# Optimization experiments

Measured on AMD Instinct MI355X. Metric: run time of the kernel, lower is better.

## Reference

```python
import jax, jax.numpy as jnp
import numpy as np
import math

B, T, D = 2, 4096, 1024
P, H, NH = 16, 64, 16  # prototypes, head_dim, num_heads
EPS = 1e-6
GAIN = 1.0
STD = 0.02

def setup_inputs() -> dict:
    key = jax.random.key(0)
    ks = jax.random.split(key, 8)
    hidden_states = jax.random.normal(ks[0], (B, T, D), jnp.float32)
    # rotary embeddings (standard HF RoPE, theta=10000)
    inv_freq = 1.0 / (10000.0 ** (np.arange(0, H, 2, dtype=np.float32) / H))
    t = np.arange(T, dtype=np.float32)
    freqs = np.outer(t, inv_freq)                     # [T, H/2]
    emb = np.concatenate([freqs, freqs], axis=-1)     # [T, H]
    cos = jnp.broadcast_to(jnp.cos(emb)[None], (B, T, H)).astype(jnp.float32)
    sin = jnp.broadcast_to(jnp.sin(emb)[None], (B, T, H)).astype(jnp.float32)
    return {
        'hidden_states': hidden_states,
        'cos': cos, 'sin': sin,
        'q_norm_w': jnp.ones((D,), jnp.float32),
        'k_proto': STD * jax.random.normal(ks[1], (P, D), jnp.float32),
        'v_proto': jnp.eye(P, dtype=jnp.float32),     # nn.init.eye_
        'q_basis': STD * jax.random.normal(ks[2], (P, D, H), jnp.float32),
        'k_basis': STD * jax.random.normal(ks[3], (P, D, H), jnp.float32),
        'v_basis': STD * jax.random.normal(ks[4], (P, D, H), jnp.float32),
        'o_w': STD * jax.random.normal(ks[5], (D, NH * H), jnp.float32),  # o_proj weight [out,in]
    }

def _rms_norm(x, w, eps=EPS):
    xf = x.astype(jnp.float32)
    var = jnp.mean(xf * xf, axis=-1, keepdims=True)
    return (xf * jax.lax.rsqrt(var + eps)).astype(x.dtype) * w

def _rotate_half(x):
    x1, x2 = jnp.split(x, 2, axis=-1)
    return jnp.concatenate([-x2, x1], axis=-1)

def reference(hidden_states, cos, sin, q_norm_w, k_proto, v_proto, q_basis, k_basis, v_basis, o_w):
    x = hidden_states
    # CAPR router
    q_r = _rms_norm(x, q_norm_w)
    aw = jax.nn.softmax(jnp.einsum('btd,pd->btp', q_r, k_proto) / math.sqrt(D), axis=-1)
    routing = jax.nn.softmax(jnp.einsum('btp,pq->btq', aw, v_proto) * GAIN, axis=-1)  # [B,T,P]
    # per-prototype projections then routing-weighted reduction over P
    # (same math as einsum('btp,pdh,btd->bth'), avoids [B,T,D,H] intermediate)
    def proj(basis):
        xp = jnp.einsum('btd,pdh->btph', x, basis)        # [B,T,P,H]
        return jnp.einsum('btp,btph->bth', routing, xp)   # [B,T,H]
    q, k, v = proj(q_basis), proj(k_basis), proj(v_basis)
    # RoPE (all num_heads copies are identical, so operate on the single head)
    q = q * cos + _rotate_half(q) * sin
    k = k * cos + _rotate_half(k) * sin
    # causal SDPA, scale = 1/sqrt(head_dim)
    scores = jnp.einsum('bqh,bkh->bqk', q, k) / math.sqrt(H)
    causal = jnp.tril(jnp.ones((T, T), bool))
    scores = jnp.where(causal[None], scores, jnp.finfo(scores.dtype).min)
    probs = jax.nn.softmax(scores, axis=-1)
    attn = jnp.einsum('bqk,bkh->bqh', probs, v)           # [B,T,H]
    # heads are expanded copies -> concat is a tile; then o_proj (no bias)
    concat = jnp.tile(attn, (1, 1, NH))                   # [B,T,NH*H]
    out = jnp.einsum('bti,oi->bto', concat, o_w)
    return out
```

## Files before the change

kernel.cpp:

```cpp
#include <hip/hip_runtime.h>

typedef __attribute__((ext_vector_type(8))) short bf16x8;
typedef __attribute__((ext_vector_type(4))) float f32x4;
typedef __attribute__((ext_vector_type(4))) unsigned short us4;

#define DEV __device__ __forceinline__

static constexpr int Bn = 2, Tn = 4096, Dn = 1024, Pn = 16, Hn = 64;
static constexpr int BT = Bn * Tn;
static constexpr int NC = 3 * Dn;
static constexpr int NUNIT = 288;

static constexpr size_t OFF_ROUTING = 0;
static constexpr size_t OFF_XBF     = OFF_ROUTING + (size_t)BT * 16 * 4;
static constexpr size_t OFF_BPK     = OFF_XBF + (size_t)BT * Dn * 2;
static constexpr size_t OFF_QKV     = OFF_BPK + (size_t)NC * Dn * 2;
static constexpr size_t OFF_QBF     = OFF_QKV + (size_t)BT * 192 * 4;
static constexpr size_t OFF_KBF     = OFF_QBF + (size_t)BT * 64 * 2;
static constexpr size_t OFF_VT      = OFF_KBF + (size_t)BT * 64 * 2;
static constexpr size_t OFF_ATTNB   = OFF_VT + (size_t)BT * 64 * 2;
static constexpr size_t OFF_OWEFF   = OFF_ATTNB + (size_t)BT * 64 * 2;

DEV unsigned short f2bf(float f) {
  unsigned int u = __builtin_bit_cast(unsigned int, f);
  u += 0x7fffu + ((u >> 16) & 1u);
  return (unsigned short)(u >> 16);
}

DEV unsigned int cvtpk(float a, float b) {
  unsigned int r;
  asm("v_cvt_pk_bf16_f32 %0, %1, %2" : "=v"(r) : "v"(a), "v"(b));
  return r;
}

DEV void gll16(const void* g, void* l) {
  __builtin_amdgcn_global_load_lds(
      (const __attribute__((address_space(1))) void*)g,
      (__attribute__((address_space(3))) void*)l, 16, 0, 0);
}

__global__ __launch_bounds__(256)
void router_kernel(const float* __restrict__ x, const float* __restrict__ w,
                   const float* __restrict__ kproto, const float* __restrict__ vproto,
                   float* __restrict__ routing, unsigned short* __restrict__ xbf)
{
  __shared__ float lgs[8][16];
  const int tid = threadIdx.x, wid = tid >> 6, lane = tid & 63;
  const int t0 = blockIdx.x * 8;

  float wv[16];
#pragma unroll
  for (int c = 0; c < 4; ++c) {
    float4 f = *(const float4*)(w + c * 256 + lane * 4);
    wv[c*4+0] = f.x; wv[c*4+1] = f.y; wv[c*4+2] = f.z; wv[c*4+3] = f.w;
  }

  float xr[2][16];
  float rs[2];
#pragma unroll
  for (int rr = 0; rr < 2; ++rr) {
    const int row = t0 + wid * 2 + rr;
    float ss = 0.f;
#pragma unroll
    for (int c = 0; c < 4; ++c) {
      float4 f = *(const float4*)(x + (size_t)row * 1024 + c * 256 + lane * 4);
      xr[rr][c*4+0] = f.x; xr[rr][c*4+1] = f.y; xr[rr][c*4+2] = f.z; xr[rr][c*4+3] = f.w;
      ss += f.x*f.x + f.y*f.y + f.z*f.z + f.w*f.w;
      us4 o; o[0] = f2bf(f.x); o[1] = f2bf(f.y); o[2] = f2bf(f.z); o[3] = f2bf(f.w);
      *(us4*)(xbf + (size_t)row * 1024 + c * 256 + lane * 4) = o;
    }
#pragma unroll
    for (int off = 1; off < 64; off <<= 1) ss += __shfl_xor(ss, off, 64);
    rs[rr] = rsqrtf(ss * (1.f / 1024.f) + 1e-6f);
  }

  for (int p = 0; p < 16; ++p) {
    float d0 = 0.f, d1 = 0.f;
#pragma unroll
    for (int c = 0; c < 4; ++c) {
      float4 f = *(const float4*)(kproto + (size_t)p * 1024 + c * 256 + lane * 4);
      float k0 = f.x * wv[c*4+0], k1 = f.y * wv[c*4+1], k2 = f.z * wv[c*4+2], k3 = f.w * wv[c*4+3];
      d0 += xr[0][c*4+0]*k0 + xr[0][c*4+1]*k1 + xr[0][c*4+2]*k2 + xr[0][c*4+3]*k3;
      d1 += xr[1][c*4+0]*k0 + xr[1][c*4+1]*k1 + xr[1][c*4+2]*k2 + xr[1][c*4+3]*k3;
    }
#pragma unroll
    for (int off = 1; off < 64; off <<= 1) {
      d0 += __shfl_xor(d0, off, 64);
      d1 += __shfl_xor(d1, off, 64);
    }
    if (lane == 0) {
      lgs[wid*2+0][p] = d0 * rs[0] * 0.03125f;
      lgs[wid*2+1][p] = d1 * rs[1] * 0.03125f;
    }
  }
  __syncthreads();
  if (tid < 8) {
    float lg[16];
#pragma unroll
    for (int p = 0; p < 16; ++p) lg[p] = lgs[tid][p];
    float m = -1e30f;
#pragma unroll
    for (int p = 0; p < 16; ++p) m = fmaxf(m, lg[p]);
    float aw[16]; float s = 0.f;
#pragma unroll
    for (int p = 0; p < 16; ++p) { aw[p] = __expf(lg[p] - m); s += aw[p]; }
    float inv = 1.f / s;
    float rt[16];
#pragma unroll
    for (int q = 0; q < 16; ++q) {
      float a = 0.f;
#pragma unroll
      for (int p = 0; p < 16; ++p) a += aw[p] * vproto[p * 16 + q];
      rt[q] = a * inv;
    }
    float m2 = -1e30f;
#pragma unroll
    for (int q = 0; q < 16; ++q) m2 = fmaxf(m2, rt[q]);
    float e[16]; float s2 = 0.f;
#pragma unroll
    for (int q = 0; q < 16; ++q) { e[q] = __expf(rt[q] - m2); s2 += e[q]; }
    float inv2 = 1.f / s2;
#pragma unroll
    for (int q = 0; q < 16; ++q) routing[(size_t)(t0 + tid) * 16 + q] = e[q] * inv2;
  }
}

__global__ __launch_bounds__(256)
void pack_bases_kernel(const float* __restrict__ qb, const float* __restrict__ kb,
                       const float* __restrict__ vb, unsigned short* __restrict__ bpk)
{
  __shared__ float tile[64][65];
  const int bid = blockIdx.x;
  const int bs = bid >> 8;
  const int p = (bid >> 4) & 15;
  const int dt = bid & 15;
  const float* src = bs == 0 ? qb : (bs == 1 ? kb : vb);
  const int tid = threadIdx.x;
#pragma unroll
  for (int j = 0; j < 4; ++j) {
    int slot = tid + j * 256;
    int r = slot >> 4;
    int c4 = slot & 15;
    float4 v = *(const float4*)(src + (size_t)p * 65536 + (size_t)(dt * 64 + r) * 64 + c4 * 4);
    tile[r][c4*4+0] = v.x; tile[r][c4*4+1] = v.y; tile[r][c4*4+2] = v.z; tile[r][c4*4+3] = v.w;
  }
  __syncthreads();
#pragma unroll
  for (int j = 0; j < 4; ++j) {
    int slot = tid + j * 256;
    int h = slot >> 4;
    int d4 = slot & 15;
    us4 o;
    o[0] = f2bf(tile[d4*4+0][h]); o[1] = f2bf(tile[d4*4+1][h]);
    o[2] = f2bf(tile[d4*4+2][h]); o[3] = f2bf(tile[d4*4+3][h]);
    int c = bs * 1024 + h * 16 + p;
    *(us4*)(bpk + (size_t)c * 1024 + dt * 64 + d4 * 4) = o;
  }
}

__global__ __launch_bounds__(256)
void pack_ow_kernel(const float* __restrict__ ow, unsigned short* __restrict__ oweff)
{
  int idx = blockIdx.x * 256 + threadIdx.x;
  int o = idx >> 6, h = idx & 63;
  float s = 0.f;
#pragma unroll
  for (int n = 0; n < 16; ++n) s += ow[(size_t)o * 1024 + n * 64 + h];
  oweff[idx] = f2bf(s);
}

__global__ __launch_bounds__(256)
void proj_gemm_kernel(const unsigned short* __restrict__ bpk,
                      const unsigned short* __restrict__ xbf,
                      const float* __restrict__ routing,
                      float* __restrict__ qkv)
{
  __shared__ __attribute__((aligned(16))) unsigned short As[2][128][64];
  __shared__ __attribute__((aligned(16))) unsigned short Bs[2][128][64];
  const int bid = blockIdx.x;
  const int swz = (bid & 7) * 192 + (bid >> 3);
  const int tt = swz / 24, ct = swz - tt * 24;
  const int c0 = ct << 7, t0 = tt << 7;
  const int tid = threadIdx.x, wid = tid >> 6, lane = tid & 63;
  const int wm = (wid >> 1) << 6, wn = (wid & 1) << 6;
  const int l15 = lane & 15, l4 = lane >> 4;
  const int sx = (l15 & 7) << 3;

  f32x4 acc[4][4];
#pragma unroll
  for (int m = 0; m < 4; ++m)
#pragma unroll
    for (int n = 0; n < 4; ++n) acc[m][n] = (f32x4){0.f, 0.f, 0.f, 0.f};

#define PROJ_STAGE(kt, pb) do {                                              \
    const int k0_ = (kt) * 64;                                               \
    const int cc_ = 8 * ((lane & 7) ^ (lane >> 3));  \
    _Pragma("unroll")                                                        \
    for (int i_ = 0; i_ < 4; ++i_) {                                         \
      int ch_ = wid * 4 + i_;                                                \
      int r_ = ch_ * 8 + (lane >> 3);                                        \
      gll16(bpk + (size_t)(c0 + r_) * 1024 + k0_ + cc_, &As[pb][ch_ * 8][0]);\
      gll16(xbf + (size_t)(t0 + r_) * 1024 + k0_ + cc_, &Bs[pb][ch_ * 8][0]);\
    } } while (0)

  PROJ_STAGE(0, 0);
  PROJ_STAGE(1, 1);

  for (int kt = 0; kt < 16; ++kt) {
    const int cb = kt & 1;
    if (kt < 15) asm volatile("s_waitcnt vmcnt(8)" ::: "memory");
    else         asm volatile("s_waitcnt vmcnt(0)" ::: "memory");
    asm volatile("s_barrier" ::: "memory");
#pragma unroll
    for (int kk = 0; kk < 2; ++kk) {
      bf16x8 af[4], bfr[4];
#pragma unroll
      for (int m = 0; m < 4; ++m)
        af[m] = *(const bf16x8*)&As[cb][wm + m * 16 + l15][(kk * 32 + l4 * 8) ^ sx];
#pragma unroll
      for (int n = 0; n < 4; ++n)
        bfr[n] = *(const bf16x8*)&Bs[cb][wn + n * 16 + l15][(kk * 32 + l4 * 8) ^ sx];
#pragma unroll
      for (int m = 0; m < 4; ++m)
#pragma unroll
        for (int n = 0; n < 4; ++n)
          acc[m][n] = __builtin_amdgcn_mfma_f32_16x16x32_bf16(af[m], bfr[n], acc[m][n], 0, 0, 0);
    }
    asm volatile("s_waitcnt lgkmcnt(0)" ::: "memory");
    asm volatile("s_barrier" ::: "memory");
    if (kt < 14) PROJ_STAGE(kt + 2, cb);
  }
#undef PROJ_STAGE

#pragma unroll
  for (int n = 0; n < 4; ++n) {
    const int t = t0 + wn + n * 16 + l15;
    const float4 rt = *(const float4*)(routing + (size_t)t * 16 + l4 * 4);
#pragma unroll
    for (int m = 0; m < 4; ++m) {
      float s = acc[m][n][0] * rt.x + acc[m][n][1] * rt.y
              + acc[m][n][2] * rt.z + acc[m][n][3] * rt.w;
      s += __shfl_xor(s, 16, 64);
      s += __shfl_xor(s, 32, 64);
      if (l4 == 0) {
        const int h16 = (c0 + wm + m * 16) >> 4;
        qkv[(size_t)t * 192 + h16] = s;
      }
    }
  }
}

__global__ __launch_bounds__(256)
void rope_kernel(const float* __restrict__ qkv, const float* __restrict__ cosb,
                 const float* __restrict__ sinb, unsigned short* __restrict__ qbf,
                 unsigned short* __restrict__ kbf, unsigned short* __restrict__ vT)
{
  constexpr float QS = 0.125f * 1.4426950408889634f;
  __shared__ float vs[64][33];
  const int tid = threadIdx.x;
  const int bt0 = blockIdx.x * 32;
  const int tokl = tid >> 3;
  const int h0 = (tid & 7) * 4;
  const size_t bt = bt0 + tokl;
  const float* base = qkv + bt * 192;
  float4 q1 = *(const float4*)(base + h0);
  float4 q2 = *(const float4*)(base + h0 + 32);
  float4 k1 = *(const float4*)(base + 64 + h0);
  float4 k2 = *(const float4*)(base + 64 + h0 + 32);
  float4 v1 = *(const float4*)(base + 128 + h0);
  float4 v2 = *(const float4*)(base + 128 + h0 + 32);
  const float* cp = cosb + bt * 64;
  const float* sp = sinb + bt * 64;
  float4 c1 = *(const float4*)(cp + h0), c2 = *(const float4*)(cp + h0 + 32);
  float4 s1 = *(const float4*)(sp + h0), s2 = *(const float4*)(sp + h0 + 32);

  us4 uq1, uq2, uk1, uk2;
  uq1[0] = f2bf((q1.x * c1.x - q2.x * s1.x) * QS);
  uq1[1] = f2bf((q1.y * c1.y - q2.y * s1.y) * QS);
  uq1[2] = f2bf((q1.z * c1.z - q2.z * s1.z) * QS);
  uq1[3] = f2bf((q1.w * c1.w - q2.w * s1.w) * QS);
  uq2[0] = f2bf((q2.x * c2.x + q1.x * s2.x) * QS);
  uq2[1] = f2bf((q2.y * c2.y + q1.y * s2.y) * QS);
  uq2[2] = f2bf((q2.z * c2.z + q1.z * s2.z) * QS);
  uq2[3] = f2bf((q2.w * c2.w + q1.w * s2.w) * QS);
  uk1[0] = f2bf(k1.x * c1.x - k2.x * s1.x);
  uk1[1] = f2bf(k1.y * c1.y - k2.y * s1.y);
  uk1[2] = f2bf(k1.z * c1.z - k2.z * s1.z);
  uk1[3] = f2bf(k1.w * c1.w - k2.w * s1.w);
  uk2[0] = f2bf(k2.x * c2.x + k1.x * s2.x);
  uk2[1] = f2bf(k2.y * c2.y + k1.y * s2.y);
  uk2[2] = f2bf(k2.z * c2.z + k1.z * s2.z);
  uk2[3] = f2bf(k2.w * c2.w + k1.w * s2.w);
  *(us4*)(qbf + bt * 64 + h0) = uq1;
  *(us4*)(qbf + bt * 64 + h0 + 32) = uq2;
  *(us4*)(kbf + bt * 64 + h0) = uk1;
  *(us4*)(kbf + bt * 64 + h0 + 32) = uk2;

  vs[h0 + 0][tokl] = v1.x; vs[h0 + 1][tokl] = v1.y; vs[h0 + 2][tokl] = v1.z; vs[h0 + 3][tokl] = v1.w;
  vs[h0 + 32][tokl] = v2.x; vs[h0 + 33][tokl] = v2.y; vs[h0 + 34][tokl] = v2.z; vs[h0 + 35][tokl] = v2.w;
  __syncthreads();
  const int h = tid >> 2, c8 = (tid & 3) * 8;
  const int b = bt0 >> 12, tb0 = bt0 & 4095;
  us4 o0, o1;
  o0[0] = f2bf(vs[h][c8 + 0]); o0[1] = f2bf(vs[h][c8 + 1]);
  o0[2] = f2bf(vs[h][c8 + 2]); o0[3] = f2bf(vs[h][c8 + 3]);
  o1[0] = f2bf(vs[h][c8 + 4]); o1[1] = f2bf(vs[h][c8 + 5]);
  o1[2] = f2bf(vs[h][c8 + 6]); o1[3] = f2bf(vs[h][c8 + 7]);
  unsigned short* vp = vT + ((size_t)b * 64 + h) * 4096 + tb0 + c8;
  *(us4*)vp = o0;
  *(us4*)(vp + 4) = o1;
}

__global__ __launch_bounds__(256)
void attn_kernel(const unsigned short* __restrict__ qbf,
                 const unsigned short* __restrict__ kbf,
                 const unsigned short* __restrict__ vT,
                 float* __restrict__ po, float* __restrict__ ml)
{
  const int bid = blockIdx.x;
  const int b = bid / NUNIT, u = bid - b * NUNIT;
  int g = 0;
  while (u >= 4 * (g + 1) * (g + 2)) ++g;
  const int r0 = u - 4 * g * (g + 1);
  const int qq = r0 / (g + 1);
  const int qt = 8 * g + qq;
  const int c = r0 - qq * (g + 1);
  const int ks = c * 512;
  const int ke = min(ks + 512, (qt + 1) * 64);

  const int tid = threadIdx.x, w = tid >> 6, lane = tid & 63;
  const int l15 = lane & 15, l4 = lane >> 4;
  const int q0w = qt * 64 + w * 16;
  const int qg = q0w + l15;

  const unsigned short* qp = qbf + (size_t)(b * 4096 + qg) * 64 + l4 * 8;
  bf16x8 qf0 = *(const bf16x8*)qp;
  bf16x8 qf1 = *(const bf16x8*)(qp + 32);

  f32x4 oacc[4];
#pragma unroll
  for (int hf = 0; hf < 4; ++hf) oacc[hf] = (f32x4){0.f, 0.f, 0.f, 0.f};
  float m = -1e30f, l = 0.f;

  const int kew = min(ke, q0w + 16);
  const int nst = (kew - ks + 63) >> 6;
  const int kperm = 8 * (l15 >> 2) + (l15 & 3);

  for (int st = 0; st < nst; ++st) {
    const int key0 = ks + st * 64;
    f32x4 s[4];
#pragma unroll
    for (int j = 0; j < 4; ++j) {
      const int krow = key0 + 32 * (j >> 1) + 4 * (j & 1) + kperm;
      const unsigned short* kp = kbf + (size_t)(b * 4096 + krow) * 64 + l4 * 8;
      bf16x8 ka = *(const bf16x8*)kp;
      bf16x8 kc = *(const bf16x8*)(kp + 32);
      f32x4 z = (f32x4){0.f, 0.f, 0.f, 0.f};
      z = __builtin_amdgcn_mfma_f32_16x16x32_bf16(ka, qf0, z, 0, 0, 0);
      s[j] = __builtin_amdgcn_mfma_f32_16x16x32_bf16(kc, qf1, z, 0, 0, 0);
    }
    bf16x8 vf[4][2];
#pragma unroll
    for (int J = 0; J < 2; ++J)
#pragma unroll
      for (int hf = 0; hf < 4; ++hf)
        vf[hf][J] = *(const bf16x8*)(vT + ((size_t)(b * 64 + hf * 16 + l15)) * 4096
                                     + key0 + J * 32 + l4 * 8);
    if (key0 + 63 > q0w) {
#pragma unroll
      for (int j = 0; j < 4; ++j) {
        const int kb0 = key0 + 32 * (j >> 1) + 4 * (j & 1) + 8 * l4;
#pragma unroll
        for (int rr = 0; rr < 4; ++rr)
          if (kb0 + rr > qg) s[j][rr] = -1e30f;
      }
    }
    float pmax = -1e30f;
#pragma unroll
    for (int j = 0; j < 4; ++j)
#pragma unroll
      for (int rr = 0; rr < 4; ++rr) pmax = fmaxf(pmax, s[j][rr]);
    pmax = fmaxf(pmax, __shfl_xor(pmax, 16, 64));
    pmax = fmaxf(pmax, __shfl_xor(pmax, 32, 64));
    const float mn = fmaxf(m, pmax);
    const float sc = __builtin_amdgcn_exp2f(m - mn);
    m = mn;
    l *= sc;
#pragma unroll
    for (int hf = 0; hf < 4; ++hf) {
      oacc[hf][0] *= sc; oacc[hf][1] *= sc; oacc[hf][2] *= sc; oacc[hf][3] *= sc;
    }
    float rs = 0.f;
    unsigned int cvw[4][2];
#pragma unroll
    for (int j = 0; j < 4; ++j) {
      const float e0 = (s[j][0] > -1e29f) ? __builtin_amdgcn_exp2f(s[j][0] - m) : 0.f;
      const float e1 = (s[j][1] > -1e29f) ? __builtin_amdgcn_exp2f(s[j][1] - m) : 0.f;
      const float e2 = (s[j][2] > -1e29f) ? __builtin_amdgcn_exp2f(s[j][2] - m) : 0.f;
      const float e3 = (s[j][3] > -1e29f) ? __builtin_amdgcn_exp2f(s[j][3] - m) : 0.f;
      rs += (e0 + e1) + (e2 + e3);
      cvw[j][0] = cvtpk(e0, e1);
      cvw[j][1] = cvtpk(e2, e3);
    }
    rs += __shfl_xor(rs, 16, 64);
    rs += __shfl_xor(rs, 32, 64);
    l += rs;
#pragma unroll
    for (int J = 0; J < 2; ++J) {
      union { unsigned int uu[4]; bf16x8 v; } pk;
      pk.uu[0] = cvw[2 * J][0];
      pk.uu[1] = cvw[2 * J][1];
      pk.uu[2] = cvw[2 * J + 1][0];
      pk.uu[3] = cvw[2 * J + 1][1];
#pragma unroll
      for (int hf = 0; hf < 4; ++hf)
        oacc[hf] = __builtin_amdgcn_mfma_f32_16x16x32_bf16(vf[hf][J], pk.v, oacc[hf], 0, 0, 0);
    }
  }

  const size_t ug = (size_t)b * NUNIT + u;
  float* pop = po + (ug * 64 + w * 16 + l15) * 64;
#pragma unroll
  for (int hf = 0; hf < 4; ++hf)
    *(f32x4*)(pop + hf * 16 + l4 * 4) = oacc[hf];
  if (l4 == 0) {
    ml[ug * 128 + w * 16 + l15] = m;
    ml[ug * 128 + 64 + w * 16 + l15] = l;
  }
}

__global__ __launch_bounds__(256)
void combine_kernel(const float* __restrict__ po, const float* __restrict__ ml,
                    unsigned short* __restrict__ attnb)
{
  const int bid = blockIdx.x;
  const int b = bid >> 6, qt = bid & 63;
  const int g = qt >> 3, r = qt & 7;
  const int nch = g + 1;
  const size_t ub = (size_t)b * NUNIT + (size_t)(g + 1) * (4 * g + r);
  const int tid = threadIdx.x;
  const int q = tid >> 2, hc = (tid & 3) * 16;

  float mt = -1e30f;
  for (int i = 0; i < nch; ++i) mt = fmaxf(mt, ml[(ub + i) * 128 + q]);
  float lt = 0.f;
  float4 a0 = {0,0,0,0}, a1 = {0,0,0,0}, a2 = {0,0,0,0}, a3 = {0,0,0,0};
  for (int i = 0; i < nch; ++i) {
    const float mi = ml[(ub + i) * 128 + q];
    const float wi = (mi > -1e29f) ? __builtin_amdgcn_exp2f(mi - mt) : 0.f;
    lt += wi * ml[(ub + i) * 128 + 64 + q];
    const float* pp = po + ((ub + i) * 64 + q) * 64 + hc;
    float4 f0 = *(const float4*)(pp + 0);
    float4 f1 = *(const float4*)(pp + 4);
    float4 f2 = *(const float4*)(pp + 8);
    float4 f3 = *(const float4*)(pp + 12);
    a0.x += wi * f0.x; a0.y += wi * f0.y; a0.z += wi * f0.z; a0.w += wi * f0.w;
    a1.x += wi * f1.x; a1.y += wi * f1.y; a1.z += wi * f1.z; a1.w += wi * f1.w;
    a2.x += wi * f2.x; a2.y += wi * f2.y; a2.z += wi * f2.z; a2.w += wi * f2.w;
    a3.x += wi * f3.x; a3.y += wi * f3.y; a3.z += wi * f3.z; a3.w += wi * f3.w;
  }
  const float inv = (lt > 0.f) ? 1.f / lt : 0.f;
  unsigned short* op = attnb + ((size_t)b * 4096 + qt * 64 + q) * 64 + hc;
  us4 o;
  o[0] = f2bf(a0.x * inv); o[1] = f2bf(a0.y * inv); o[2] = f2bf(a0.z * inv); o[3] = f2bf(a0.w * inv);
  *(us4*)(op + 0) = o;
  o[0] = f2bf(a1.x * inv); o[1] = f2bf(a1.y * inv); o[2] = f2bf(a1.z * inv); o[3] = f2bf(a1.w * inv);
  *(us4*)(op + 4) = o;
  o[0] = f2bf(a2.x * inv); o[1] = f2bf(a2.y * inv); o[2] = f2bf(a2.z * inv); o[3] = f2bf(a2.w * inv);
  *(us4*)(op + 8) = o;
  o[0] = f2bf(a3.x * inv); o[1] = f2bf(a3.y * inv); o[2] = f2bf(a3.z * inv); o[3] = f2bf(a3.w * inv);
  *(us4*)(op + 12) = o;
}

__global__ __launch_bounds__(256)
void oproj_kernel(const unsigned short* __restrict__ attnb,
                  const unsigned short* __restrict__ oweff,
                  float* __restrict__ out)
{
  __shared__ __attribute__((aligned(16))) unsigned short As[128][64];
  __shared__ __attribute__((aligned(16))) unsigned short Bs[128][64];
  const int bid = blockIdx.x;
  const int swz = (bid & 7) * 64 + (bid >> 3);
  const int mt = swz >> 3, nt = swz & 7;
  const int m0 = mt << 7, n0 = nt << 7;
  const int tid = threadIdx.x, wid = tid >> 6, lane = tid & 63;
  const int wm = (wid >> 1) << 6, wn = (wid & 1) << 6;
  const int l15 = lane & 15, l4 = lane >> 4;

#pragma unroll
  for (int i = 0; i < 4; ++i) {
    int ch = wid * 4 + i;
    int r = ch * 8 + (lane >> 3), c = (lane & 7) * 8;
    gll16(attnb + (size_t)(m0 + r) * 64 + c, &As[ch * 8][0]);
    gll16(oweff + (size_t)(n0 + r) * 64 + c, &Bs[ch * 8][0]);
  }
  __syncthreads();

  f32x4 acc[4][4];
#pragma unroll
  for (int m = 0; m < 4; ++m)
#pragma unroll
    for (int n = 0; n < 4; ++n) acc[m][n] = (f32x4){0.f, 0.f, 0.f, 0.f};
#pragma unroll
  for (int kk = 0; kk < 2; ++kk) {
    bf16x8 af[4], bfr[4];
#pragma unroll
    for (int m = 0; m < 4; ++m) af[m] = *(const bf16x8*)&As[wm + m * 16 + l15][kk * 32 + l4 * 8];
#pragma unroll
    for (int n = 0; n < 4; ++n) bfr[n] = *(const bf16x8*)&Bs[wn + n * 16 + l15][kk * 32 + l4 * 8];
#pragma unroll
    for (int m = 0; m < 4; ++m)
#pragma unroll
      for (int n = 0; n < 4; ++n)
        acc[m][n] = __builtin_amdgcn_mfma_f32_16x16x32_bf16(af[m], bfr[n], acc[m][n], 0, 0, 0);
  }
#pragma unroll
  for (int m = 0; m < 4; ++m)
#pragma unroll
    for (int n = 0; n < 4; ++n)
#pragma unroll
      for (int r = 0; r < 4; ++r)
        out[(size_t)(m0 + wm + m * 16 + l4 * 4 + r) * 1024 + n0 + wn + n * 16 + l15] = acc[m][n][r];
}

extern "C" void kernel_launch(void* const* d_in, const int* in_sizes, int n_in,
                              void* d_out, int out_size, void* d_ws, size_t ws_size,
                              hipStream_t stream) {
  const float* x      = (const float*)d_in[0];
  const float* cosb   = (const float*)d_in[1];
  const float* sinb   = (const float*)d_in[2];
  const float* qw     = (const float*)d_in[3];
  const float* kproto = (const float*)d_in[4];
  const float* vproto = (const float*)d_in[5];
  const float* qb     = (const float*)d_in[6];
  const float* kb     = (const float*)d_in[7];
  const float* vb     = (const float*)d_in[8];
  const float* ow     = (const float*)d_in[9];
  float* out = (float*)d_out;
  char* ws = (char*)d_ws;

  float* routing        = (float*)(ws + OFF_ROUTING);
  unsigned short* xbf   = (unsigned short*)(ws + OFF_XBF);
  unsigned short* bpk   = (unsigned short*)(ws + OFF_BPK);
  float* qkv            = (float*)(ws + OFF_QKV);
  unsigned short* qbf   = (unsigned short*)(ws + OFF_QBF);
  unsigned short* kbf   = (unsigned short*)(ws + OFF_KBF);
  unsigned short* vT    = (unsigned short*)(ws + OFF_VT);
  unsigned short* attnb = (unsigned short*)(ws + OFF_ATTNB);
  unsigned short* oweff = (unsigned short*)(ws + OFF_OWEFF);
  float* po             = (float*)(ws + OFF_XBF);
  float* ml             = (float*)(ws + OFF_BPK);

  router_kernel<<<BT / 8, 256, 0, stream>>>(x, qw, kproto, vproto, routing, xbf);
  pack_bases_kernel<<<768, 256, 0, stream>>>(qb, kb, vb, bpk);
  pack_ow_kernel<<<256, 256, 0, stream>>>(ow, oweff);
  proj_gemm_kernel<<<1536, 256, 0, stream>>>(bpk, xbf, routing, qkv);
  rope_kernel<<<BT / 32, 256, 0, stream>>>(qkv, cosb, sinb, qbf, kbf, vT);
  attn_kernel<<<Bn * NUNIT, 256, 0, stream>>>(qbf, kbf, vT, po, ml);
  combine_kernel<<<128, 256, 0, stream>>>(po, ml, attnb);
  oproj_kernel<<<512, 256, 0, stream>>>(attnb, oweff, out);
}
```

Before: 152.0 us.

## Merge prep kernels and enlarge projection GEMM tile with triple buffering

```diff
diff --git a/kernel.cpp b/kernel.cpp
--- a/kernel.cpp
+++ b/kernel.cpp
@@ -40,151 +40,152 @@
 }
 
 __global__ __launch_bounds__(256)
-void router_kernel(const float* __restrict__ x, const float* __restrict__ w,
-                   const float* __restrict__ kproto, const float* __restrict__ vproto,
-                   float* __restrict__ routing, unsigned short* __restrict__ xbf)
+void prep_kernel(const float* __restrict__ x, const float* __restrict__ w,
+                 const float* __restrict__ kproto, const float* __restrict__ vproto,
+                 const float* __restrict__ qb, const float* __restrict__ kb,
+                 const float* __restrict__ vb, const float* __restrict__ ow,
+                 float* __restrict__ routing, unsigned short* __restrict__ xbf,
+                 unsigned short* __restrict__ bpk, unsigned short* __restrict__ oweff)
 {
   __shared__ float lgs[8][16];
-  const int tid = threadIdx.x, wid = tid >> 6, lane = tid & 63;
-  const int t0 = blockIdx.x * 8;
-
-  float wv[16];
-#pragma unroll
-  for (int c = 0; c < 4; ++c) {
-    float4 f = *(const float4*)(w + c * 256 + lane * 4);
-    wv[c*4+0] = f.x; wv[c*4+1] = f.y; wv[c*4+2] = f.z; wv[c*4+3] = f.w;
-  }
-
-  float xr[2][16];
-  float rs[2];
-#pragma unroll
-  for (int rr = 0; rr < 2; ++rr) {
-    const int row = t0 + wid * 2 + rr;
-    float ss = 0.f;
-#pragma unroll
-    for (int c = 0; c < 4; ++c) {
-      float4 f = *(const float4*)(x + (size_t)row * 1024 + c * 256 + lane * 4);
-      xr[rr][c*4+0] = f.x; xr[rr][c*4+1] = f.y; xr[rr][c*4+2] = f.z; xr[rr][c*4+3] = f.w;
-      ss += f.x*f.x + f.y*f.y + f.z*f.z + f.w*f.w;
-      us4 o; o[0] = f2bf(f.x); o[1] = f2bf(f.y); o[2] = f2bf(f.z); o[3] = f2bf(f.w);
-      *(us4*)(xbf + (size_t)row * 1024 + c * 256 + lane * 4) = o;
-    }
-#pragma unroll
-    for (int off = 1; off < 64; off <<= 1) ss += __shfl_xor(ss, off, 64);
-    rs[rr] = rsqrtf(ss * (1.f / 1024.f) + 1e-6f);
-  }
-
-  for (int p = 0; p < 16; ++p) {
-    float d0 = 0.f, d1 = 0.f;
-#pragma unroll
-    for (int c = 0; c < 4; ++c) {
-      float4 f = *(const float4*)(kproto + (size_t)p * 1024 + c * 256 + lane * 4);
-      float k0 = f.x * wv[c*4+0], k1 = f.y * wv[c*4+1], k2 = f.z * wv[c*4+2], k3 = f.w * wv[c*4+3];
-      d0 += xr[0][c*4+0]*k0 + xr[0][c*4+1]*k1 + xr[0][c*4+2]*k2 + xr[0][c*4+3]*k3;
-      d1 += xr[1][c*4+0]*k0 + xr[1][c*4+1]*k1 + xr[1][c*4+2]*k2 + xr[1][c*4+3]*k3;
-    }
-#pragma unroll
-    for (int off = 1; off < 64; off <<= 1) {
-      d0 += __shfl_xor(d0, off, 64);
-      d1 += __shfl_xor(d1, off, 64);
-    }
-    if (lane == 0) {
-      lgs[wid*2+0][p] = d0 * rs[0] * 0.03125f;
-      lgs[wid*2+1][p] = d1 * rs[1] * 0.03125f;
-    }
-  }
-  __syncthreads();
-  if (tid < 8) {
-    float lg[16];
-#pragma unroll
-    for (int p = 0; p < 16; ++p) lg[p] = lgs[tid][p];
-    float m = -1e30f;
-#pragma unroll
-    for (int p = 0; p < 16; ++p) m = fmaxf(m, lg[p]);
-    float aw[16]; float s = 0.f;
-#pragma unroll
-    for (int p = 0; p < 16; ++p) { aw[p] = __expf(lg[p] - m); s += aw[p]; }
-    float inv = 1.f / s;
-    float rt[16];
-#pragma unroll
-    for (int q = 0; q < 16; ++q) {
-      float a = 0.f;
-#pragma unroll
-      for (int p = 0; p < 16; ++p) a += aw[p] * vproto[p * 16 + q];
-      rt[q] = a * inv;
-    }
-    float m2 = -1e30f;
-#pragma unroll
-    for (int q = 0; q < 16; ++q) m2 = fmaxf(m2, rt[q]);
-    float e[16]; float s2 = 0.f;
-#pragma unroll
-    for (int q = 0; q < 16; ++q) { e[q] = __expf(rt[q] - m2); s2 += e[q]; }
-    float inv2 = 1.f / s2;
-#pragma unroll
-    for (int q = 0; q < 16; ++q) routing[(size_t)(t0 + tid) * 16 + q] = e[q] * inv2;
-  }
-}
-
-__global__ __launch_bounds__(256)
-void pack_bases_kernel(const float* __restrict__ qb, const float* __restrict__ kb,
-                       const float* __restrict__ vb, unsigned short* __restrict__ bpk)
-{
   __shared__ float tile[64][65];
   const int bid = blockIdx.x;
-  const int bs = bid >> 8;
-  const int p = (bid >> 4) & 15;
-  const int dt = bid & 15;
-  const float* src = bs == 0 ? qb : (bs == 1 ? kb : vb);
   const int tid = threadIdx.x;
-#pragma unroll
-  for (int j = 0; j < 4; ++j) {
-    int slot = tid + j * 256;
-    int r = slot >> 4;
-    int c4 = slot & 15;
-    float4 v = *(const float4*)(src + (size_t)p * 65536 + (size_t)(dt * 64 + r) * 64 + c4 * 4);
-    tile[r][c4*4+0] = v.x; tile[r][c4*4+1] = v.y; tile[r][c4*4+2] = v.z; tile[r][c4*4+3] = v.w;
-  }
-  __syncthreads();
-#pragma unroll
-  for (int j = 0; j < 4; ++j) {
-    int slot = tid + j * 256;
-    int h = slot >> 4;
-    int d4 = slot & 15;
-    us4 o;
-    o[0] = f2bf(tile[d4*4+0][h]); o[1] = f2bf(tile[d4*4+1][h]);
-    o[2] = f2bf(tile[d4*4+2][h]); o[3] = f2bf(tile[d4*4+3][h]);
-    int c = bs * 1024 + h * 16 + p;
-    *(us4*)(bpk + (size_t)c * 1024 + dt * 64 + d4 * 4) = o;
-  }
-}
-
-__global__ __launch_bounds__(256)
-void pack_ow_kernel(const float* __restrict__ ow, unsigned short* __restrict__ oweff)
-{
-  int idx = blockIdx.x * 256 + threadIdx.x;
-  int o = idx >> 6, h = idx & 63;
-  float s = 0.f;
-#pragma unroll
-  for (int n = 0; n < 16; ++n) s += ow[(size_t)o * 1024 + n * 64 + h];
-  oweff[idx] = f2bf(s);
-}
-
-__global__ __launch_bounds__(256)
+
+  if (bid < 1024) {
+    const int wid = tid >> 6, lane = tid & 63;
+    const int t0 = bid * 8;
+
+    float wv[16];
+#pragma unroll
+    for (int c = 0; c < 4; ++c) {
+      float4 f = *(const float4*)(w + c * 256 + lane * 4);
+      wv[c*4+0] = f.x; wv[c*4+1] = f.y; wv[c*4+2] = f.z; wv[c*4+3] = f.w;
+    }
+
+    float xr[2][16];
+    float rs[2];
+#pragma unroll
+    for (int rr = 0; rr < 2; ++rr) {
+      const int row = t0 + wid * 2 + rr;
+      float ss = 0.f;
+#pragma unroll
+      for (int c = 0; c < 4; ++c) {
+        float4 f = *(const float4*)(x + (size_t)row * 1024 + c * 256 + lane * 4);
+        xr[rr][c*4+0] = f.x; xr[rr][c*4+1] = f.y; xr[rr][c*4+2] = f.z; xr[rr][c*4+3] = f.w;
+        ss += f.x*f.x + f.y*f.y + f.z*f.z + f.w*f.w;
+        us4 o; o[0] = f2bf(f.x); o[1] = f2bf(f.y); o[2] = f2bf(f.z); o[3] = f2bf(f.w);
+        *(us4*)(xbf + (size_t)row * 1024 + c * 256 + lane * 4) = o;
+      }
+#pragma unroll
+      for (int off = 1; off < 64; off <<= 1) ss += __shfl_xor(ss, off, 64);
+      rs[rr] = rsqrtf(ss * (1.f / 1024.f) + 1e-6f);
+    }
+
+    for (int p = 0; p < 16; ++p) {
+      float d0 = 0.f, d1 = 0.f;
+#pragma unroll
+      for (int c = 0; c < 4; ++c) {
+        float4 f = *(const float4*)(kproto + (size_t)p * 1024 + c * 256 + lane * 4);
+        float k0 = f.x * wv[c*4+0], k1 = f.y * wv[c*4+1], k2 = f.z * wv[c*4+2], k3 = f.w * wv[c*4+3];
+        d0 += xr[0][c*4+0]*k0 + xr[0][c*4+1]*k1 + xr[0][c*4+2]*k2 + xr[0][c*4+3]*k3;
+        d1 += xr[1][c*4+0]*k0 + xr[1][c*4+1]*k1 + xr[1][c*4+2]*k2 + xr[1][c*4+3]*k3;
+      }
+#pragma unroll
+      for (int off = 1; off < 64; off <<= 1) {
+        d0 += __shfl_xor(d0, off, 64);
+        d1 += __shfl_xor(d1, off, 64);
+      }
+      if (lane == 0) {
+        lgs[wid*2+0][p] = d0 * rs[0] * 0.03125f;
+        lgs[wid*2+1][p] = d1 * rs[1] * 0.03125f;
+      }
+    }
+    __syncthreads();
+    if (tid < 8) {
+      float lg[16];
+#pragma unroll
+      for (int p = 0; p < 16; ++p) lg[p] = lgs[tid][p];
+      float m = -1e30f;
+#pragma unroll
+      for (int p = 0; p < 16; ++p) m = fmaxf(m, lg[p]);
+      float aw[16]; float s = 0.f;
+#pragma unroll
+      for (int p = 0; p < 16; ++p) { aw[p] = __expf(lg[p] - m); s += aw[p]; }
+      float inv = 1.f / s;
+      float rt[16];
+#pragma unroll
+      for (int q = 0; q < 16; ++q) {
+        float a = 0.f;
+#pragma unroll
+        for (int p = 0; p < 16; ++p) a += aw[p] * vproto[p * 16 + q];
+        rt[q] = a * inv;
+      }
+      float m2 = -1e30f;
+#pragma unroll
+      for (int q = 0; q < 16; ++q) m2 = fmaxf(m2, rt[q]);
+      float e[16]; float s2 = 0.f;
+#pragma unroll
+      for (int q = 0; q < 16; ++q) { e[q] = __expf(rt[q] - m2); s2 += e[q]; }
+      float inv2 = 1.f / s2;
+#pragma unroll
+      for (int q = 0; q < 16; ++q) routing[(size_t)(t0 + tid) * 16 + q] = e[q] * inv2;
+    }
+  } else if (bid < 1792) {
+    const int pbid = bid - 1024;
+    const int bs = pbid >> 8;
+    const int p = (pbid >> 4) & 15;
+    const int dt = pbid & 15;
+    const float* src = bs == 0 ? qb : (bs == 1 ? kb : vb);
+#pragma unroll
+    for (int j = 0; j < 4; ++j) {
+      int slot = tid + j * 256;
+      int r = slot >> 4;
+      int c4 = slot & 15;
+      float4 v = *(const float4*)(src + (size_t)p * 65536 + (size_t)(dt * 64 + r) * 64 + c4 * 4);
+      tile[r][c4*4+0] = v.x; tile[r][c4*4+1] = v.y; tile[r][c4*4+2] = v.z; tile[r][c4*4+3] = v.w;
+    }
+    __syncthreads();
+#pragma unroll
+    for (int j = 0; j < 4; ++j) {
+      int slot = tid + j * 256;
+      int h = slot >> 4;
+      int d4 = slot & 15;
+      us4 o;
+      o[0] = f2bf(tile[d4*4+0][h]); o[1] = f2bf(tile[d4*4+1][h]);
+      o[2] = f2bf(tile[d4*4+2][h]); o[3] = f2bf(tile[d4*4+3][h]);
+      int c = bs * 1024 + h * 16 + p;
+      *(us4*)(bpk + (size_t)c * 1024 + dt * 64 + d4 * 4) = o;
+    }
+  } else {
+    int idx = (bid - 1792) * 256 + tid;
+    int o = idx >> 6, h = idx & 63;
+    float s = 0.f;
+#pragma unroll
+    for (int n = 0; n < 16; ++n) s += ow[(size_t)o * 1024 + n * 64 + h];
+    oweff[idx] = f2bf(s);
+  }
+}
+
+__global__ __launch_bounds__(512, 2)
 void proj_gemm_kernel(const unsigned short* __restrict__ bpk,
                       const unsigned short* __restrict__ xbf,
                       const float* __restrict__ routing,
                       float* __restrict__ qkv)
 {
-  __shared__ __attribute__((aligned(16))) unsigned short As[2][128][64];
-  __shared__ __attribute__((aligned(16))) unsigned short Bs[2][128][64];
+  __shared__ __attribute__((aligned(16))) unsigned short As[3][128][64];
+  __shared__ __attribute__((aligned(16))) unsigned short Bs[3][256][64];
   const int bid = blockIdx.x;
-  const int swz = (bid & 7) * 192 + (bid >> 3);
+  const int swz = (bid & 7) * 96 + (bid >> 3);
   const int tt = swz / 24, ct = swz - tt * 24;
-  const int c0 = ct << 7, t0 = tt << 7;
+  const int c0 = ct << 7, t0 = tt << 8;
   const int tid = threadIdx.x, wid = tid >> 6, lane = tid & 63;
-  const int wm = (wid >> 1) << 6, wn = (wid & 1) << 6;
+  const int wm = (wid >> 2) << 6;
+  const int wn = (wid & 3) << 6;
   const int l15 = lane & 15, l4 = lane >> 4;
   const int sx = (l15 & 7) << 3;
+  const int trow = tid >> 3;
+  const int ccs = 8 * ((lane & 7) ^ ((lane >> 3) & 7));
 
   f32x4 acc[4][4];
 #pragma unroll
@@ -192,24 +193,25 @@
 #pragma unroll
     for (int n = 0; n < 4; ++n) acc[m][n] = (f32x4){0.f, 0.f, 0.f, 0.f};
 
-#define PROJ_STAGE(kt, pb) do {                                              \
-    const int k0_ = (kt) * 64;                                               \
-    const int cc_ = 8 * ((lane & 7) ^ (lane >> 3));  \
-    _Pragma("unroll")                                                        \
-    for (int i_ = 0; i_ < 4; ++i_) {                                         \
-      int ch_ = wid * 4 + i_;                                                \
-      int r_ = ch_ * 8 + (lane >> 3);                                        \
-      gll16(bpk + (size_t)(c0 + r_) * 1024 + k0_ + cc_, &As[pb][ch_ * 8][0]);\
-      gll16(xbf + (size_t)(t0 + r_) * 1024 + k0_ + cc_, &Bs[pb][ch_ * 8][0]);\
-    } } while (0)
+#define PROJ_STAGE(kt, pb) do {                                                   \
+    const int k0_ = (kt) * 64;                                                    \
+    gll16(bpk + (size_t)(c0 + trow) * 1024 + k0_ + ccs,       &As[pb][wid * 8][0]);        \
+    gll16(bpk + (size_t)(c0 + 64 + trow) * 1024 + k0_ + ccs,  &As[pb][64 + wid * 8][0]);   \
+    gll16(xbf + (size_t)(t0 + trow) * 1024 + k0_ + ccs,       &Bs[pb][wid * 8][0]);        \
+    gll16(xbf + (size_t)(t0 + 64 + trow) * 1024 + k0_ + ccs,  &Bs[pb][64 + wid * 8][0]);   \
+    gll16(xbf + (size_t)(t0 + 128 + trow) * 1024 + k0_ + ccs, &Bs[pb][128 + wid * 8][0]);  \
+    gll16(xbf + (size_t)(t0 + 192 + trow) * 1024 + k0_ + ccs, &Bs[pb][192 + wid * 8][0]);  \
+  } while (0)
 
   PROJ_STAGE(0, 0);
   PROJ_STAGE(1, 1);
-
+  PROJ_STAGE(2, 2);
+
+  int cb = 0;
   for (int kt = 0; kt < 16; ++kt) {
-    const int cb = kt & 1;
-    if (kt < 15) asm volatile("s_waitcnt vmcnt(8)" ::: "memory");
-    else         asm volatile("s_waitcnt vmcnt(0)" ::: "memory");
+    if (kt <= 13)      asm volatile("s_waitcnt vmcnt(12)" ::: "memory");
+    else if (kt == 14) asm volatile("s_waitcnt vmcnt(6)" ::: "memory");
+    else               asm volatile("s_waitcnt vmcnt(0)" ::: "memory");
     asm volatile("s_barrier" ::: "memory");
 #pragma unroll
     for (int kk = 0; kk < 2; ++kk) {
@@ -228,7 +230,8 @@
     }
     asm volatile("s_waitcnt lgkmcnt(0)" ::: "memory");
     asm volatile("s_barrier" ::: "memory");
-    if (kt < 14) PROJ_STAGE(kt + 2, cb);
+    if (kt < 13) PROJ_STAGE(kt + 3, cb);
+    cb = (cb == 2) ? 0 : cb + 1;
   }
 #undef PROJ_STAGE
 
@@ -551,10 +554,9 @@
   float* po             = (float*)(ws + OFF_XBF);
   float* ml             = (float*)(ws + OFF_BPK);
 
-  router_kernel<<<BT / 8, 256, 0, stream>>>(x, qw, kproto, vproto, routing, xbf);
-  pack_bases_kernel<<<768, 256, 0, stream>>>(qb, kb, vb, bpk);
-  pack_ow_kernel<<<256, 256, 0, stream>>>(ow, oweff);
-  proj_gemm_kernel<<<1536, 256, 0, stream>>>(bpk, xbf, routing, qkv);
+  prep_kernel<<<2048, 256, 0, stream>>>(x, qw, kproto, vproto, qb, kb, vb, ow,
+                                        routing, xbf, bpk, oweff);
+  proj_gemm_kernel<<<768, 512, 0, stream>>>(bpk, xbf, routing, qkv);
   rope_kernel<<<BT / 32, 256, 0, stream>>>(qkv, cosb, sinb, qbf, kbf, vT);
   attn_kernel<<<Bn * NUNIT, 256, 0, stream>>>(qbf, kbf, vT, po, ml);
   combine_kernel<<<128, 256, 0, stream>>>(po, ml, attnb);
```

Result: slower. 158.1 us (+4.0%).
